# Optimization experiments

Hardware: AMD Instinct MI355X
Metric: run time of the kernel (lower is better)

## Reference

```python
import math
import jax, jax.numpy as jnp
import numpy as np
from jax import lax

B = 4; N = 4096; F = 15; A = 24          # batch, tcr_num, feature_num, aa_num
HID = 10; H = 1; HD = 10; AFN = 14       # attn hidden, heads, head dim, sum(filter_num)
KS = [2, 3, 4, 5, 6, 7]; FN = [3, 3, 3, 2, 2, 1]
K = int(N * 0.05)                        # routing topk = 204
SCALE = np.float32(1.0 / math.sqrt(HD))


def setup_inputs() -> dict:
    key = jax.random.key(0)
    ks = jax.random.split(key, 24)
    inp = {"x": jax.random.normal(ks[0], (B, N, F, A), jnp.float32)}
    for i, (h, f) in enumerate(zip(KS, FN)):
        inp["conv_w%d" % h] = jax.random.normal(ks[1 + 2 * i], (f, F, h), jnp.float32) * 0.1
        inp["conv_b%d" % h] = jax.random.normal(ks[2 + 2 * i], (f,), jnp.float32) * 0.1
    specs = [("q", HID, AFN), ("k", HID, AFN), ("v", HID, AFN), ("attn", AFN, HID), ("mil", 2, AFN)]
    for j, (nm, o, i_) in enumerate(specs):
        inp["w_" + nm] = jax.random.normal(ks[13 + 2 * j], (o, i_), jnp.float32) * 0.1
        inp["b_" + nm] = jax.random.normal(ks[14 + 2 * j], (o,), jnp.float32) * 0.1
    return inp


def reference(x, conv_w2, conv_b2, conv_w3, conv_b3, conv_w4, conv_b4,
              conv_w5, conv_b5, conv_w6, conv_b6, conv_w7, conv_b7,
              w_q, b_q, w_k, b_k, w_v, b_v, w_attn, b_attn, w_mil, b_mil):
    # --- per-sequence conv feature extraction ---
    xc = x.reshape(-1, F, A)  # [B*N, 15, 24]
    feats = []
    for w, b in [(conv_w2, conv_b2), (conv_w3, conv_b3), (conv_w4, conv_b4),
                 (conv_w5, conv_b5), (conv_w6, conv_b6), (conv_w7, conv_b7)]:
        y = lax.conv_general_dilated(xc, w, (1,), 'VALID',
                                     dimension_numbers=('NCH', 'OIH', 'NCH'))
        y = jax.nn.relu(y + b[None, :, None])
        feats.append(jnp.max(y, axis=-1))  # AdaptiveMaxPool1d(1)
    out = jnp.concatenate(feats, axis=1).reshape(B, N, AFN)  # [B, N, 14]

    # --- QKV projections, split into heads -> [B, H, N, HD] ---
    q = (out @ w_q.T + b_q).reshape(B, N, H, HD).transpose(0, 2, 1, 3)
    k = (out @ w_k.T + b_k).reshape(B, N, H, HD).transpose(0, 2, 1, 3)
    v = (out @ w_v.T + b_v).reshape(B, N, H, HD).transpose(0, 2, 1, 3)

    # --- bi-level routing: full scores, topk over head-mean (detached in torch) ---
    scores_raw = jnp.einsum('bhnd,bhmd->bhnm', q, k)  # [B, H, N, N]
    a_r = jnp.mean(lax.stop_gradient(scores_raw), axis=1)  # [B, N, N]
    _, idx = lax.top_k(a_r, K)  # [B, N, K] int32
    idx_r = jnp.broadcast_to(idx[:, None], (B, H, N, K))

    scores = jnp.take_along_axis(scores_raw * SCALE, idx_r, axis=3)  # [B, H, N, K]
    # gather values per (batch, head, query): v_g[b,h,i,j] = v[b,h,idx[b,h,i,j]]
    v_g = jax.vmap(jax.vmap(lambda vh, ih: vh[ih]))(v, idx_r)  # [B, H, N, K, HD]

    probs = jax.nn.softmax(scores, axis=-1)  # dropout is identity at p=0 / eval
    ctx = jnp.einsum('bhnk,bhnkd->bhnd', probs, v_g)  # [B, H, N, HD]
    ctx = ctx.transpose(0, 2, 1, 3).reshape(B, N, HID)

    ctx = ctx @ w_attn.T + b_attn          # [B, N, 14]
    logits = ctx @ w_mil.T + b_mil          # [B, N, 2]
    pooled = jnp.sum(logits, axis=1) / N    # [B, 2]
    return pooled, probs[:, :, :, None, :]  # probs shaped [B, H, N, 1, K] as in torch
```

## Files before the change

### kernel.cpp

```cpp
#include <hip/hip_runtime.h>
#include <math.h>

#define NB 4
#define NN 4096
#define KSEL 204
#define NBINS 512
#define CANDN 256
#define QKSCALE 0.31622776601683794f

#define WS_Q 0
#define WS_KT (NB * NN * 10)
#define WS_V (2 * NB * NN * 10)
#define WS_LG (3 * NB * NN * 10)

#define SEQ_PER_BLOCK 16

typedef float v2f __attribute__((ext_vector_type(2)));


__global__ __launch_bounds__(256) void featqkv_kernel(
    const float* __restrict__ x,
    const float* __restrict__ w2, const float* __restrict__ b2,
    const float* __restrict__ w3, const float* __restrict__ b3,
    const float* __restrict__ w4, const float* __restrict__ b4,
    const float* __restrict__ w5, const float* __restrict__ b5,
    const float* __restrict__ w6, const float* __restrict__ b6,
    const float* __restrict__ w7, const float* __restrict__ b7,
    const float* __restrict__ wq, const float* __restrict__ bq,
    const float* __restrict__ wk, const float* __restrict__ bk,
    const float* __restrict__ wv, const float* __restrict__ bv,
    float* __restrict__ q_out, float* __restrict__ kT_out, float* __restrict__ v_out)
{
    __shared__ __align__(16) float xs[SEQ_PER_BLOCK * 360];
    __shared__ float wpad[14 * 105];
    __shared__ float bconv[14];
    __shared__ float wqkv[420];
    __shared__ float bqkv[30];
    __shared__ float feats[SEQ_PER_BLOCK * 14];

    const int t = threadIdx.x;
    const int g0 = blockIdx.x * SEQ_PER_BLOCK;

    {
        const float4* xg4 = reinterpret_cast<const float4*>(x + (size_t)g0 * 360);
        float4* xs4 = reinterpret_cast<float4*>(xs);
        for (int i = t; i < SEQ_PER_BLOCK * 90; i += 256) xs4[i] = xg4[i];
    }

    for (int i = t; i < 14 * 105; i += 256) {
        const int ch = i / 105;
        const int r = i - ch * 105;
        const int c = r / 7;
        const int j = r - (r / 7) * 7;
        float val = 0.f;
        if (ch < 3)       { if (j < 2) val = w2[ch * 30 + c * 2 + j]; }
        else if (ch < 6)  { if (j < 3) val = w3[(ch - 3) * 45 + c * 3 + j]; }
        else if (ch < 9)  { if (j < 4) val = w4[(ch - 6) * 60 + c * 4 + j]; }
        else if (ch < 11) { if (j < 5) val = w5[(ch - 9) * 75 + c * 5 + j]; }
        else if (ch < 13) { if (j < 6) val = w6[(ch - 11) * 90 + c * 6 + j]; }
        else              { val = w7[c * 7 + j]; }
        wpad[i] = val;
    }
    if (t < 3) bconv[t] = b2[t];
    else if (t < 6) bconv[t] = b3[t - 3];
    else if (t < 9) bconv[t] = b4[t - 6];
    else if (t < 11) bconv[t] = b5[t - 9];
    else if (t < 13) bconv[t] = b6[t - 11];
    else if (t == 13) bconv[t] = b7[0];
    for (int i = t; i < 140; i += 256) wqkv[i] = wq[i];
    for (int i = t; i < 140; i += 256) wqkv[140 + i] = wk[i];
    for (int i = t; i < 140; i += 256) wqkv[280 + i] = wv[i];
    if (t < 10) bqkv[t] = bq[t];
    else if (t < 20) bqkv[t] = bk[t - 10];
    else if (t < 30) bqkv[t] = bv[t - 20];
    __syncthreads();

    const int seq = t >> 4;
    const int wkr = t & 15;

    if (wkr < 14) {
        const int ch = wkr;
        int T;
        if (ch < 3) T = 23; else if (ch < 6) T = 22; else if (ch < 9) T = 21;
        else if (ch < 11) T = 20; else if (ch < 13) T = 19; else T = 18;

        float acc[23];
#pragma unroll
        for (int u = 0; u < 23; u++) acc[u] = 0.f;
        const float* xrow = &xs[seq * 360];
        const float* wrow = &wpad[ch * 105];
        for (int c = 0; c < 15; c++) {
            float xr[30];
            const float4* xp = reinterpret_cast<const float4*>(xrow + c * 24);
#pragma unroll
            for (int u4 = 0; u4 < 6; u4++) {
                const float4 xv = xp[u4];
                xr[u4 * 4 + 0] = xv.x; xr[u4 * 4 + 1] = xv.y;
                xr[u4 * 4 + 2] = xv.z; xr[u4 * 4 + 3] = xv.w;
            }
#pragma unroll
            for (int u = 24; u < 30; u++) xr[u] = 0.f;
#pragma unroll
            for (int j = 0; j < 7; j++) {
                const float wv_ = wrow[c * 7 + j];
#pragma unroll
                for (int tt = 0; tt < 23; tt++)
                    acc[tt] = fmaf(xr[tt + j], wv_, acc[tt]);
            }
        }
        float m = -3.0e38f;
#pragma unroll
        for (int tt = 0; tt < 23; tt++)
            if (tt < T) m = fmaxf(m, acc[tt]);
        feats[seq * 14 + ch] = fmaxf(m + bconv[ch], 0.f);
    }
    __syncthreads();

    const int g = g0 + seq;
    const int b_ = g >> 12;
    const int n_ = g & 4095;
    for (int o = wkr; o < 30; o += 16) {
        const int type = o / 10;
        const int comp = o % 10;
        const float* wrow = &wqkv[type * 140 + comp * 14];
        const float* frow = &feats[seq * 14];
        float a = bqkv[type * 10 + comp];
#pragma unroll
        for (int ii = 0; ii < 14; ii++) a = fmaf(frow[ii], wrow[ii], a);
        if (type == 0) q_out[(size_t)g * 10 + comp] = a;
        else if (type == 1) kT_out[((size_t)b_ * 10 + comp) * NN + n_] = a;
        else v_out[(size_t)g * 10 + comp] = a;
    }
}

__device__ __forceinline__ float dec_key(unsigned int k) {
    return (k & 0x80000000u) ? __uint_as_float(k ^ 0x80000000u)
                             : __uint_as_float(~k);
}
__device__ __forceinline__ unsigned int enc_key(float s) {
    unsigned int u = __float_as_uint(s);
    return (u & 0x80000000u) ? ~u : (u | 0x80000000u);
}

__global__ __launch_bounds__(256, 8) void attn_kernel(
    const float* __restrict__ qbuf, const float* __restrict__ kTbuf,
    const float* __restrict__ vbuf,
    const float* __restrict__ w_attn, const float* __restrict__ b_attn,
    const float* __restrict__ w_mil, const float* __restrict__ b_mil,
    float* __restrict__ out_probs, float* __restrict__ logits)
{
    __shared__ unsigned int base_[NBINS];
    __shared__ unsigned int bc_[NBINS];
    __shared__ unsigned long long cand[CANDN];
    __shared__ float hpart[4], lpart[4], fpart[4];
    __shared__ unsigned int wtot[4];
    __shared__ float ctxp[40];

    const int t = threadIdx.x;
    const int lane = t & 63;
    const int w = t >> 6;
    const int row = blockIdx.x;
    const int b_ = row >> 12;

    float q0, q1, q2, q3, q4, q5, q6, q7, q8, q9;
    {
        const float* qp = qbuf + (size_t)row * 10;
        q0 = qp[0]; q1 = qp[1]; q2 = qp[2]; q3 = qp[3]; q4 = qp[4];
        q5 = qp[5]; q6 = qp[6]; q7 = qp[7]; q8 = qp[8]; q9 = qp[9];
    }
    const float* kTb = kTbuf + (size_t)b_ * 10 * NN;
    float sc[16];
    float vhi = -1e30f, vlo = 1e30f;
#pragma unroll
    for (int i = 0; i < 4; i++) {
        v2f a01 = {0.f, 0.f};
        v2f a23 = {0.f, 0.f};
#pragma unroll
        for (int c = 0; c < 10; c++) {
            const float qc = (c == 0) ? q0 : (c == 1) ? q1 : (c == 2) ? q2 : (c == 3) ? q3 :
                             (c == 4) ? q4 : (c == 5) ? q5 : (c == 6) ? q6 : (c == 7) ? q7 :
                             (c == 8) ? q8 : q9;
            const float4 kv = reinterpret_cast<const float4*>(kTb + c * NN)[i * 256 + t];
            v2f kxy; kxy.x = kv.x; kxy.y = kv.y;
            v2f kzw; kzw.x = kv.z; kzw.y = kv.w;
            v2f qv; qv.x = qc; qv.y = qc;
            a01 = __builtin_elementwise_fma(qv, kxy, a01);
            a23 = __builtin_elementwise_fma(qv, kzw, a23);
        }
        sc[i * 4 + 0] = a01.x; sc[i * 4 + 1] = a01.y;
        sc[i * 4 + 2] = a23.x; sc[i * 4 + 3] = a23.y;
        vhi = fmaxf(vhi, fmaxf(fmaxf(a01.x, a01.y), fmaxf(a23.x, a23.y)));
        vlo = fminf(vlo, fminf(fminf(a01.x, a01.y), fminf(a23.x, a23.y)));
    }
#pragma unroll
    for (int off = 32; off > 0; off >>= 1) {
        vhi = fmaxf(vhi, __shfl_xor(vhi, off));
        vlo = fminf(vlo, __shfl_xor(vlo, off));
    }
    if (lane == 0) { hpart[w] = vhi; lpart[w] = vlo; }
    base_[2 * t] = 0u; base_[2 * t + 1] = 0u;
    cand[t] = 0ULL;
    __syncthreads();
    const float hi = fmaxf(fmaxf(hpart[0], hpart[1]), fmaxf(hpart[2], hpart[3]));
    const float lo = fminf(fminf(lpart[0], lpart[1]), fminf(lpart[2], lpart[3]));
    const bool degen = (hi <= lo);

    float pv = 0.f;
    int jj = 0, p = KSEL;
    bool selected = false;
    const float smax = hi * QKSCALE;

    if (!degen) {
        const float scale = (float)(NBINS - 1) / (hi - lo);

        int bins[16];
#pragma unroll
        for (int i = 0; i < 16; i++) {
            const int bin = (int)fminf((sc[i] - lo) * scale, (float)(NBINS - 1));
            bins[i] = bin;
            atomicAdd(&base_[bin], 1u);
        }
        __syncthreads();

        {
            const unsigned int c0 = base_[2 * t];
            const unsigned int c1 = base_[2 * t + 1];
            const unsigned int T_ = c0 + c1;
            unsigned int acc = T_;
#pragma unroll
            for (int off = 1; off < 64; off <<= 1) {
                unsigned int o = __shfl_down(acc, off);
                if (lane + off < 64) acc += o;
            }
            if (lane == 0) wtot[w] = acc;
            __syncthreads();
            unsigned int tail = 0u;
#pragma unroll
            for (int w2 = 1; w2 < 4; w2++) if (w2 > w) tail += wtot[w2];
            const unsigned int A = (acc - T_) + tail;
            base_[2 * t + 1] = A;
            base_[2 * t] = A + c1;
            bc_[2 * t + 1] = A;
            bc_[2 * t] = A + c1;
        }
        __syncthreads();

#pragma unroll
        for (int i = 0; i < 16; i++) {
            const int bin = bins[i];
            const unsigned int bs = base_[bin];
            if (bs < KSEL) {
                const unsigned int pos = atomicAdd(&bc_[bin], 1u);
                if (pos < CANDN) {
                    const int j = (i >> 2) * 1024 + t * 4 + (i & 3);
                    cand[pos] = (((unsigned long long)enc_key(sc[i])) << 16)
                              | (unsigned long long)(4095 - j);
                }
            }
        }
        __syncthreads();

        const unsigned long long mine = cand[t];
        if (mine != 0ULL) {
            const float s = dec_key((unsigned int)(mine >> 16));
            const int bin = (int)fminf((s - lo) * scale, (float)(NBINS - 1));
            const unsigned int bs = base_[bin];
            unsigned int e2 = (bin > 0) ? base_[bin - 1] : 4096u;
            if (e2 > CANDN) e2 = CANDN;
            unsigned int rank = 0;
            for (unsigned int s2 = bs; s2 < e2; s2++)
                rank += (cand[s2] > mine) ? 1u : 0u;
            const unsigned int pp = bs + rank;
            if (pp < KSEL) {
                selected = true;
                p = (int)pp;
                jj = 4095 - (int)(mine & 0xFFFFu);
                pv = expf(s * QKSCALE - smax);
            }
        }
    } else {
        if (t < KSEL) {
            selected = true;
            p = t;
            jj = t;
            pv = 1.f;
        }
    }

    float cx0 = 0.f, cx1 = 0.f, cx2 = 0.f, cx3 = 0.f, cx4 = 0.f;
    float cx5 = 0.f, cx6 = 0.f, cx7 = 0.f, cx8 = 0.f, cx9 = 0.f;
    if (selected) {
        const float* vr = vbuf + ((size_t)b_ * NN + (size_t)jj) * 10;
        const float2 v01 = reinterpret_cast<const float2*>(vr)[0];
        const float2 v23 = reinterpret_cast<const float2*>(vr)[1];
        const float2 v45 = reinterpret_cast<const float2*>(vr)[2];
        const float2 v67 = reinterpret_cast<const float2*>(vr)[3];
        const float2 v89 = reinterpret_cast<const float2*>(vr)[4];
        cx0 = pv * v01.x; cx1 = pv * v01.y;
        cx2 = pv * v23.x; cx3 = pv * v23.y;
        cx4 = pv * v45.x; cx5 = pv * v45.y;
        cx6 = pv * v67.x; cx7 = pv * v67.y;
        cx8 = pv * v89.x; cx9 = pv * v89.y;
    }
    float dsum = pv;
#pragma unroll
    for (int off = 32; off > 0; off >>= 1) {
        dsum += __shfl_xor(dsum, off);
        cx0 += __shfl_xor(cx0, off); cx1 += __shfl_xor(cx1, off);
        cx2 += __shfl_xor(cx2, off); cx3 += __shfl_xor(cx3, off);
        cx4 += __shfl_xor(cx4, off); cx5 += __shfl_xor(cx5, off);
        cx6 += __shfl_xor(cx6, off); cx7 += __shfl_xor(cx7, off);
        cx8 += __shfl_xor(cx8, off); cx9 += __shfl_xor(cx9, off);
    }
    if (lane == 0) {
        fpart[w] = dsum;
        ctxp[w * 10 + 0] = cx0; ctxp[w * 10 + 1] = cx1; ctxp[w * 10 + 2] = cx2;
        ctxp[w * 10 + 3] = cx3; ctxp[w * 10 + 4] = cx4; ctxp[w * 10 + 5] = cx5;
        ctxp[w * 10 + 6] = cx6; ctxp[w * 10 + 7] = cx7; ctxp[w * 10 + 8] = cx8;
        ctxp[w * 10 + 9] = cx9;
    }
    __syncthreads();
    const float inv = 1.f / (fpart[0] + fpart[1] + fpart[2] + fpart[3]);

    if (selected) out_probs[(size_t)row * KSEL + p] = pv * inv;

    if (w == 0) {
        float m0 = 0.f, m1 = 0.f;
        if (lane < 14) {
            float a = b_attn[lane];
#pragma unroll
            for (int d = 0; d < 10; d++) {
                const float ctxd = (ctxp[d] + ctxp[10 + d] + ctxp[20 + d] + ctxp[30 + d]) * inv;
                a = fmaf(ctxd, w_attn[lane * 10 + d], a);
            }
            m0 = a * w_mil[lane];
            m1 = a * w_mil[14 + lane];
        }
#pragma unroll
        for (int off = 8; off > 0; off >>= 1) {
            m0 += __shfl_xor(m0, off);
            m1 += __shfl_xor(m1, off);
        }
        if (lane == 0) {
            float2 lgv;
            lgv.x = m0 + b_mil[0];
            lgv.y = m1 + b_mil[1];
            *reinterpret_cast<float2*>(logits + (size_t)row * 2) = lgv;
        }
    }
}

__global__ __launch_bounds__(256) void pool_kernel(
    const float* __restrict__ logits, float* __restrict__ out)
{
    __shared__ float red[256];
    const int t = threadIdx.x;
    const int bc = blockIdx.x;
    const int b_ = bc >> 1;
    const int c_ = bc & 1;
    float a = 0.f;
    for (int n2 = t; n2 < NN; n2 += 256)
        a += logits[((size_t)b_ * NN + n2) * 2 + c_];
    red[t] = a;
    __syncthreads();
    for (int off = 128; off > 0; off >>= 1) {
        if (t < off) red[t] += red[t + off];
        __syncthreads();
    }
    if (t == 0) out[bc] = red[0] * (1.f / 4096.f);
}

extern "C" void kernel_launch(void* const* d_in, const int* in_sizes, int n_in,
                              void* d_out, int out_size, void* d_ws, size_t ws_size,
                              hipStream_t stream) {
    const float* x  = (const float*)d_in[0];
    const float* w2 = (const float*)d_in[1];  const float* b2 = (const float*)d_in[2];
    const float* w3 = (const float*)d_in[3];  const float* b3 = (const float*)d_in[4];
    const float* w4 = (const float*)d_in[5];  const float* b4 = (const float*)d_in[6];
    const float* w5 = (const float*)d_in[7];  const float* b5 = (const float*)d_in[8];
    const float* w6 = (const float*)d_in[9];  const float* b6 = (const float*)d_in[10];
    const float* w7 = (const float*)d_in[11]; const float* b7 = (const float*)d_in[12];
    const float* wq = (const float*)d_in[13]; const float* bq = (const float*)d_in[14];
    const float* wk = (const float*)d_in[15]; const float* bk = (const float*)d_in[16];
    const float* wv = (const float*)d_in[17]; const float* bv = (const float*)d_in[18];
    const float* wat = (const float*)d_in[19]; const float* bat = (const float*)d_in[20];
    const float* wm = (const float*)d_in[21];  const float* bm = (const float*)d_in[22];

    float* ws = (float*)d_ws;
    float* qb = ws + WS_Q;
    float* kT = ws + WS_KT;
    float* vb = ws + WS_V;
    float* lg = ws + WS_LG;
    float* out = (float*)d_out;

    hipLaunchKernelGGL(featqkv_kernel, dim3(NB * NN / SEQ_PER_BLOCK), dim3(256), 0, stream,
                       x, w2, b2, w3, b3, w4, b4, w5, b5, w6, b6, w7, b7,
                       wq, bq, wk, bk, wv, bv, qb, kT, vb);
    hipLaunchKernelGGL(attn_kernel, dim3(NB * NN), dim3(256), 0, stream,
                       qb, kT, vb, wat, bat, wm, bm, out + 8, lg);
    hipLaunchKernelGGL(pool_kernel, dim3(8), dim3(256), 0, stream, lg, out);
}
```

Measured before the change: 260.6 us.

## Process two query rows per 512-thread attention block to reuse K loads

```diff
diff --git a/kernel.cpp b/kernel.cpp
--- a/kernel.cpp
+++ b/kernel.cpp
@@ -14,8 +14,6 @@
 #define WS_LG (3 * NB * NN * 10)
 
 #define SEQ_PER_BLOCK 16
-
-typedef float v2f __attribute__((ext_vector_type(2)));
 
 
 __global__ __launch_bounds__(256) void featqkv_kernel(
@@ -142,7 +140,7 @@
     return (u & 0x80000000u) ? ~u : (u | 0x80000000u);
 }
 
-__global__ __launch_bounds__(256, 8) void attn_kernel(
+__global__ __launch_bounds__(512) void attn_kernel(
     const float* __restrict__ qbuf, const float* __restrict__ kTbuf,
     const float* __restrict__ vbuf,
     const float* __restrict__ w_attn, const float* __restrict__ b_attn,
@@ -152,186 +150,208 @@
     __shared__ unsigned int base_[NBINS];
     __shared__ unsigned int bc_[NBINS];
     __shared__ unsigned long long cand[CANDN];
-    __shared__ float hpart[4], lpart[4], fpart[4];
-    __shared__ unsigned int wtot[4];
-    __shared__ float ctxp[40];
+    __shared__ float hpart[2][8], lpart[2][8], fpart[2][8];
+    __shared__ unsigned int wtot[8];
+    __shared__ float ctxp[2][8][10];
 
     const int t = threadIdx.x;
     const int lane = t & 63;
     const int w = t >> 6;
-    const int row = blockIdx.x;
-    const int b_ = row >> 12;
-
-    float q0, q1, q2, q3, q4, q5, q6, q7, q8, q9;
+    const int r0 = blockIdx.x * 2;
+    const int b_ = r0 >> 12;
+
+    float qr[2][10];
     {
-        const float* qp = qbuf + (size_t)row * 10;
-        q0 = qp[0]; q1 = qp[1]; q2 = qp[2]; q3 = qp[3]; q4 = qp[4];
-        q5 = qp[5]; q6 = qp[6]; q7 = qp[7]; q8 = qp[8]; q9 = qp[9];
-    }
+        const float2* qp2 = reinterpret_cast<const float2*>(qbuf + (size_t)r0 * 10);
+        float2 v[10];
+#pragma unroll
+        for (int i = 0; i < 10; i++) v[i] = qp2[i];
+#pragma unroll
+        for (int i = 0; i < 5; i++) { qr[0][2 * i] = v[i].x; qr[0][2 * i + 1] = v[i].y; }
+#pragma unroll
+        for (int i = 0; i < 5; i++) { qr[1][2 * i] = v[5 + i].x; qr[1][2 * i + 1] = v[5 + i].y; }
+    }
+
     const float* kTb = kTbuf + (size_t)b_ * 10 * NN;
-    float sc[16];
-    float vhi = -1e30f, vlo = 1e30f;
-#pragma unroll
-    for (int i = 0; i < 4; i++) {
-        v2f a01 = {0.f, 0.f};
-        v2f a23 = {0.f, 0.f};
+    float sc[2][8];
+    float vhi0 = -1e30f, vlo0 = 1e30f, vhi1 = -1e30f, vlo1 = 1e30f;
+#pragma unroll
+    for (int g = 0; g < 2; g++) {
+        float a0x = 0.f, a0y = 0.f, a0z = 0.f, a0w = 0.f;
+        float a1x = 0.f, a1y = 0.f, a1z = 0.f, a1w = 0.f;
 #pragma unroll
         for (int c = 0; c < 10; c++) {
-            const float qc = (c == 0) ? q0 : (c == 1) ? q1 : (c == 2) ? q2 : (c == 3) ? q3 :
-                             (c == 4) ? q4 : (c == 5) ? q5 : (c == 6) ? q6 : (c == 7) ? q7 :
-                             (c == 8) ? q8 : q9;
-            const float4 kv = reinterpret_cast<const float4*>(kTb + c * NN)[i * 256 + t];
-            v2f kxy; kxy.x = kv.x; kxy.y = kv.y;
-            v2f kzw; kzw.x = kv.z; kzw.y = kv.w;
-            v2f qv; qv.x = qc; qv.y = qc;
-            a01 = __builtin_elementwise_fma(qv, kxy, a01);
-            a23 = __builtin_elementwise_fma(qv, kzw, a23);
-        }
-        sc[i * 4 + 0] = a01.x; sc[i * 4 + 1] = a01.y;
-        sc[i * 4 + 2] = a23.x; sc[i * 4 + 3] = a23.y;
-        vhi = fmaxf(vhi, fmaxf(fmaxf(a01.x, a01.y), fmaxf(a23.x, a23.y)));
-        vlo = fminf(vlo, fminf(fminf(a01.x, a01.y), fminf(a23.x, a23.y)));
+            const float4 kv = reinterpret_cast<const float4*>(kTb + c * NN)[g * 512 + t];
+            a0x = fmaf(qr[0][c], kv.x, a0x);
+            a0y = fmaf(qr[0][c], kv.y, a0y);
+            a0z = fmaf(qr[0][c], kv.z, a0z);
+            a0w = fmaf(qr[0][c], kv.w, a0w);
+            a1x = fmaf(qr[1][c], kv.x, a1x);
+            a1y = fmaf(qr[1][c], kv.y, a1y);
+            a1z = fmaf(qr[1][c], kv.z, a1z);
+            a1w = fmaf(qr[1][c], kv.w, a1w);
+        }
+        sc[0][g * 4 + 0] = a0x; sc[0][g * 4 + 1] = a0y;
+        sc[0][g * 4 + 2] = a0z; sc[0][g * 4 + 3] = a0w;
+        sc[1][g * 4 + 0] = a1x; sc[1][g * 4 + 1] = a1y;
+        sc[1][g * 4 + 2] = a1z; sc[1][g * 4 + 3] = a1w;
+        vhi0 = fmaxf(vhi0, fmaxf(fmaxf(a0x, a0y), fmaxf(a0z, a0w)));
+        vlo0 = fminf(vlo0, fminf(fminf(a0x, a0y), fminf(a0z, a0w)));
+        vhi1 = fmaxf(vhi1, fmaxf(fmaxf(a1x, a1y), fmaxf(a1z, a1w)));
+        vlo1 = fminf(vlo1, fminf(fminf(a1x, a1y), fminf(a1z, a1w)));
     }
 #pragma unroll
     for (int off = 32; off > 0; off >>= 1) {
-        vhi = fmaxf(vhi, __shfl_xor(vhi, off));
-        vlo = fminf(vlo, __shfl_xor(vlo, off));
-    }
-    if (lane == 0) { hpart[w] = vhi; lpart[w] = vlo; }
-    base_[2 * t] = 0u; base_[2 * t + 1] = 0u;
-    cand[t] = 0ULL;
-    __syncthreads();
-    const float hi = fmaxf(fmaxf(hpart[0], hpart[1]), fmaxf(hpart[2], hpart[3]));
-    const float lo = fminf(fminf(lpart[0], lpart[1]), fminf(lpart[2], lpart[3]));
-    const bool degen = (hi <= lo);
-
-    float pv = 0.f;
-    int jj = 0, p = KSEL;
-    bool selected = false;
-    const float smax = hi * QKSCALE;
-
-    if (!degen) {
-        const float scale = (float)(NBINS - 1) / (hi - lo);
-
-        int bins[16];
-#pragma unroll
-        for (int i = 0; i < 16; i++) {
-            const int bin = (int)fminf((sc[i] - lo) * scale, (float)(NBINS - 1));
-            bins[i] = bin;
-            atomicAdd(&base_[bin], 1u);
-        }
+        vhi0 = fmaxf(vhi0, __shfl_xor(vhi0, off));
+        vlo0 = fminf(vlo0, __shfl_xor(vlo0, off));
+        vhi1 = fmaxf(vhi1, __shfl_xor(vhi1, off));
+        vlo1 = fminf(vlo1, __shfl_xor(vlo1, off));
+    }
+    if (lane == 0) {
+        hpart[0][w] = vhi0; lpart[0][w] = vlo0;
+        hpart[1][w] = vhi1; lpart[1][w] = vlo1;
+    }
+
+#pragma unroll
+    for (int rr = 0; rr < 2; rr++) {
+        base_[t] = 0u;
+        if (t < CANDN) cand[t] = 0ULL;
         __syncthreads();
 
-        {
-            const unsigned int c0 = base_[2 * t];
-            const unsigned int c1 = base_[2 * t + 1];
-            const unsigned int T_ = c0 + c1;
-            unsigned int acc = T_;
-#pragma unroll
-            for (int off = 1; off < 64; off <<= 1) {
-                unsigned int o = __shfl_down(acc, off);
-                if (lane + off < 64) acc += o;
-            }
-            if (lane == 0) wtot[w] = acc;
+        const float hi = fmaxf(fmaxf(fmaxf(hpart[rr][0], hpart[rr][1]),
+                                     fmaxf(hpart[rr][2], hpart[rr][3])),
+                               fmaxf(fmaxf(hpart[rr][4], hpart[rr][5]),
+                                     fmaxf(hpart[rr][6], hpart[rr][7])));
+        const float lo = fminf(fminf(fminf(lpart[rr][0], lpart[rr][1]),
+                                     fminf(lpart[rr][2], lpart[rr][3])),
+                               fminf(fminf(lpart[rr][4], lpart[rr][5]),
+                                     fminf(lpart[rr][6], lpart[rr][7])));
+        const bool degen = (hi <= lo);
+        const float smax = hi * QKSCALE;
+
+        float pv = 0.f;
+        int jj = 0, p = KSEL;
+        bool selected = false;
+
+        if (!degen) {
+            const float scale = (float)(NBINS - 1) / (hi - lo);
+
+#pragma unroll
+            for (int i = 0; i < 8; i++) {
+                const int bin = (int)fminf((sc[rr][i] - lo) * scale, (float)(NBINS - 1));
+                atomicAdd(&base_[bin], 1u);
+            }
             __syncthreads();
-            unsigned int tail = 0u;
-#pragma unroll
-            for (int w2 = 1; w2 < 4; w2++) if (w2 > w) tail += wtot[w2];
-            const unsigned int A = (acc - T_) + tail;
-            base_[2 * t + 1] = A;
-            base_[2 * t] = A + c1;
-            bc_[2 * t + 1] = A;
-            bc_[2 * t] = A + c1;
+
+            {
+                const unsigned int c0 = base_[t];
+                unsigned int acc = c0;
+#pragma unroll
+                for (int off = 1; off < 64; off <<= 1) {
+                    unsigned int o = __shfl_down(acc, off);
+                    if (lane + off < 64) acc += o;
+                }
+                if (lane == 0) wtot[w] = acc;
+                __syncthreads();
+                unsigned int tail = 0u;
+#pragma unroll
+                for (int w2 = 1; w2 < 8; w2++) if (w2 > w) tail += wtot[w2];
+                const unsigned int A = (acc - c0) + tail;
+                base_[t] = A;
+                bc_[t] = A;
+            }
+            __syncthreads();
+
+#pragma unroll
+            for (int i = 0; i < 8; i++) {
+                const int bin = (int)fminf((sc[rr][i] - lo) * scale, (float)(NBINS - 1));
+                const unsigned int bs = base_[bin];
+                if (bs < KSEL) {
+                    const unsigned int pos = atomicAdd(&bc_[bin], 1u);
+                    if (pos < CANDN) {
+                        const int j = (i >> 2) * 2048 + t * 4 + (i & 3);
+                        cand[pos] = (((unsigned long long)enc_key(sc[rr][i])) << 16)
+                                  | (unsigned long long)(4095 - j);
+                    }
+                }
+            }
+            __syncthreads();
+
+            if (t < CANDN) {
+                const unsigned long long mine = cand[t];
+                if (mine != 0ULL) {
+                    const float s = dec_key((unsigned int)(mine >> 16));
+                    const int bin = (int)fminf((s - lo) * scale, (float)(NBINS - 1));
+                    const unsigned int bs = base_[bin];
+                    unsigned int e2 = (bin > 0) ? base_[bin - 1] : 4096u;
+                    if (e2 > CANDN) e2 = CANDN;
+                    unsigned int rank = 0;
+                    for (unsigned int s2 = bs; s2 < e2; s2++)
+                        rank += (cand[s2] > mine) ? 1u : 0u;
+                    const unsigned int pq = bs + rank;
+                    if (pq < KSEL) {
+                        selected = true;
+                        p = (int)pq;
+                        jj = 4095 - (int)(mine & 0xFFFFu);
+                        pv = expf(s * QKSCALE - smax);
+                    }
+                }
+            }
+        } else {
+            if (t < KSEL) { selected = true; p = t; jj = t; pv = 1.f; }
+        }
+
+        float cx0 = 0.f, cx1 = 0.f, cx2 = 0.f, cx3 = 0.f, cx4 = 0.f;
+        float cx5 = 0.f, cx6 = 0.f, cx7 = 0.f, cx8 = 0.f, cx9 = 0.f;
+        if (selected) {
+            const float* vr = vbuf + ((size_t)b_ * NN + (size_t)jj) * 10;
+            const float2 v01 = reinterpret_cast<const float2*>(vr)[0];
+            const float2 v23 = reinterpret_cast<const float2*>(vr)[1];
+            const float2 v45 = reinterpret_cast<const float2*>(vr)[2];
+            const float2 v67 = reinterpret_cast<const float2*>(vr)[3];
+            const float2 v89 = reinterpret_cast<const float2*>(vr)[4];
+            cx0 = pv * v01.x; cx1 = pv * v01.y;
+            cx2 = pv * v23.x; cx3 = pv * v23.y;
+            cx4 = pv * v45.x; cx5 = pv * v45.y;
+            cx6 = pv * v67.x; cx7 = pv * v67.y;
+            cx8 = pv * v89.x; cx9 = pv * v89.y;
+        }
+        float dsum = pv;
+#pragma unroll
+        for (int off = 32; off > 0; off >>= 1) {
+            dsum += __shfl_xor(dsum, off);
+            cx0 += __shfl_xor(cx0, off); cx1 += __shfl_xor(cx1, off);
+            cx2 += __shfl_xor(cx2, off); cx3 += __shfl_xor(cx3, off);
+            cx4 += __shfl_xor(cx4, off); cx5 += __shfl_xor(cx5, off);
+            cx6 += __shfl_xor(cx6, off); cx7 += __shfl_xor(cx7, off);
+            cx8 += __shfl_xor(cx8, off); cx9 += __shfl_xor(cx9, off);
+        }
+        if (lane == 0) {
+            fpart[rr][w] = dsum;
+            ctxp[rr][w][0] = cx0; ctxp[rr][w][1] = cx1; ctxp[rr][w][2] = cx2;
+            ctxp[rr][w][3] = cx3; ctxp[rr][w][4] = cx4; ctxp[rr][w][5] = cx5;
+            ctxp[rr][w][6] = cx6; ctxp[rr][w][7] = cx7; ctxp[rr][w][8] = cx8;
+            ctxp[rr][w][9] = cx9;
         }
         __syncthreads();
-
-#pragma unroll
-        for (int i = 0; i < 16; i++) {
-            const int bin = bins[i];
-            const unsigned int bs = base_[bin];
-            if (bs < KSEL) {
-                const unsigned int pos = atomicAdd(&bc_[bin], 1u);
-                if (pos < CANDN) {
-                    const int j = (i >> 2) * 1024 + t * 4 + (i & 3);
-                    cand[pos] = (((unsigned long long)enc_key(sc[i])) << 16)
-                              | (unsigned long long)(4095 - j);
-                }
-            }
-        }
-        __syncthreads();
-
-        const unsigned long long mine = cand[t];
-        if (mine != 0ULL) {
-            const float s = dec_key((unsigned int)(mine >> 16));
-            const int bin = (int)fminf((s - lo) * scale, (float)(NBINS - 1));
-            const unsigned int bs = base_[bin];
-            unsigned int e2 = (bin > 0) ? base_[bin - 1] : 4096u;
-            if (e2 > CANDN) e2 = CANDN;
-            unsigned int rank = 0;
-            for (unsigned int s2 = bs; s2 < e2; s2++)
-                rank += (cand[s2] > mine) ? 1u : 0u;
-            const unsigned int pp = bs + rank;
-            if (pp < KSEL) {
-                selected = true;
-                p = (int)pp;
-                jj = 4095 - (int)(mine & 0xFFFFu);
-                pv = expf(s * QKSCALE - smax);
-            }
-        }
-    } else {
-        if (t < KSEL) {
-            selected = true;
-            p = t;
-            jj = t;
-            pv = 1.f;
-        }
-    }
-
-    float cx0 = 0.f, cx1 = 0.f, cx2 = 0.f, cx3 = 0.f, cx4 = 0.f;
-    float cx5 = 0.f, cx6 = 0.f, cx7 = 0.f, cx8 = 0.f, cx9 = 0.f;
-    if (selected) {
-        const float* vr = vbuf + ((size_t)b_ * NN + (size_t)jj) * 10;
-        const float2 v01 = reinterpret_cast<const float2*>(vr)[0];
-        const float2 v23 = reinterpret_cast<const float2*>(vr)[1];
-        const float2 v45 = reinterpret_cast<const float2*>(vr)[2];
-        const float2 v67 = reinterpret_cast<const float2*>(vr)[3];
-        const float2 v89 = reinterpret_cast<const float2*>(vr)[4];
-        cx0 = pv * v01.x; cx1 = pv * v01.y;
-        cx2 = pv * v23.x; cx3 = pv * v23.y;
-        cx4 = pv * v45.x; cx5 = pv * v45.y;
-        cx6 = pv * v67.x; cx7 = pv * v67.y;
-        cx8 = pv * v89.x; cx9 = pv * v89.y;
-    }
-    float dsum = pv;
-#pragma unroll
-    for (int off = 32; off > 0; off >>= 1) {
-        dsum += __shfl_xor(dsum, off);
-        cx0 += __shfl_xor(cx0, off); cx1 += __shfl_xor(cx1, off);
-        cx2 += __shfl_xor(cx2, off); cx3 += __shfl_xor(cx3, off);
-        cx4 += __shfl_xor(cx4, off); cx5 += __shfl_xor(cx5, off);
-        cx6 += __shfl_xor(cx6, off); cx7 += __shfl_xor(cx7, off);
-        cx8 += __shfl_xor(cx8, off); cx9 += __shfl_xor(cx9, off);
-    }
-    if (lane == 0) {
-        fpart[w] = dsum;
-        ctxp[w * 10 + 0] = cx0; ctxp[w * 10 + 1] = cx1; ctxp[w * 10 + 2] = cx2;
-        ctxp[w * 10 + 3] = cx3; ctxp[w * 10 + 4] = cx4; ctxp[w * 10 + 5] = cx5;
-        ctxp[w * 10 + 6] = cx6; ctxp[w * 10 + 7] = cx7; ctxp[w * 10 + 8] = cx8;
-        ctxp[w * 10 + 9] = cx9;
-    }
-    __syncthreads();
-    const float inv = 1.f / (fpart[0] + fpart[1] + fpart[2] + fpart[3]);
-
-    if (selected) out_probs[(size_t)row * KSEL + p] = pv * inv;
-
-    if (w == 0) {
+        const float inv = 1.f / (fpart[rr][0] + fpart[rr][1] + fpart[rr][2] + fpart[rr][3]
+                               + fpart[rr][4] + fpart[rr][5] + fpart[rr][6] + fpart[rr][7]);
+        if (selected) out_probs[(size_t)(r0 + rr) * KSEL + p] = pv * inv;
+    }
+
+    if (w < 2) {
+        const int rr = w;
+        const float invr = 1.f / (fpart[rr][0] + fpart[rr][1] + fpart[rr][2] + fpart[rr][3]
+                                + fpart[rr][4] + fpart[rr][5] + fpart[rr][6] + fpart[rr][7]);
         float m0 = 0.f, m1 = 0.f;
         if (lane < 14) {
             float a = b_attn[lane];
 #pragma unroll
             for (int d = 0; d < 10; d++) {
-                const float ctxd = (ctxp[d] + ctxp[10 + d] + ctxp[20 + d] + ctxp[30 + d]) * inv;
-                a = fmaf(ctxd, w_attn[lane * 10 + d], a);
+                float ctxd = 0.f;
+#pragma unroll
+                for (int w2 = 0; w2 < 8; w2++) ctxd += ctxp[rr][w2][d];
+                a = fmaf(ctxd * invr, w_attn[lane * 10 + d], a);
             }
             m0 = a * w_mil[lane];
             m1 = a * w_mil[14 + lane];
@@ -345,7 +365,7 @@
             float2 lgv;
             lgv.x = m0 + b_mil[0];
             lgv.y = m1 + b_mil[1];
-            *reinterpret_cast<float2*>(logits + (size_t)row * 2) = lgv;
+            *reinterpret_cast<float2*>(logits + (size_t)(r0 + rr) * 2) = lgv;
         }
     }
 }
@@ -396,7 +416,7 @@
     hipLaunchKernelGGL(featqkv_kernel, dim3(NB * NN / SEQ_PER_BLOCK), dim3(256), 0, stream,
                        x, w2, b2, w3, b3, w4, b4, w5, b5, w6, b6, w7, b7,
                        wq, bq, wk, bk, wv, bv, qb, kT, vb);
-    hipLaunchKernelGGL(attn_kernel, dim3(NB * NN), dim3(256), 0, stream,
+    hipLaunchKernelGGL(attn_kernel, dim3(NB * NN / 2), dim3(512), 0, stream,
                        qb, kT, vb, wat, bat, wm, bm, out + 8, lg);
     hipLaunchKernelGGL(pool_kernel, dim3(8), dim3(256), 0, stream, lg, out);
 }
```

New measurement: 334.1 us. +28.2%, slower.
